# Performance work log

Hardware: AMD Instinct MI355X
Metric: run time of the kernel (lower is better)

The kernel has to match this reference:

```python
import jax, jax.numpy as jnp
import numpy as np

DIM = 384; H = 56; W = 56; WS = 7; SHIFT = 3; NH = 12; B = 32
N = WS * WS                 # 49 tokens per window
NW = (H // WS) * (W // WS)  # 64 windows per image
HD = DIM // NH
EPS = 1e-5


def _rel_coords_table():
    c = np.arange(-(WS - 1), WS, dtype=np.float32)
    hh, ww = np.meshgrid(c, c, indexing='ij')
    t = np.stack([hh, ww], -1)[None]          # (1, 2*WS-1, 2*WS-1, 2)
    t = t / (WS - 1) * 8.0
    t = np.sign(t) * np.log2(np.abs(t) + 1.0) / 3.0
    return t.astype(np.float32)


def _rel_pos_index():
    coords = np.stack(np.meshgrid(np.arange(WS), np.arange(WS), indexing='ij'))  # (2,WS,WS)
    cf = coords.reshape(2, -1)
    rc = (cf[:, :, None] - cf[:, None, :]).transpose(1, 2, 0)  # (N,N,2)
    rc[..., 0] += WS - 1
    rc[..., 1] += WS - 1
    rc[..., 0] *= 2 * WS - 1
    return rc.sum(-1)  # (N,N) int


def _attn_mask():
    img = np.zeros((H, W))
    sl = [slice(0, -WS), slice(-WS, -SHIFT), slice(-SHIFT, None)]
    cnt = 0
    for hs in sl:
        for ws in sl:
            img[hs, ws] = cnt
            cnt += 1
    mw = img.reshape(H // WS, WS, W // WS, WS).transpose(0, 2, 1, 3).reshape(-1, N)
    diff = mw[:, None, :] - mw[:, :, None]  # (NW, N, N)
    return np.where(diff != 0, -100.0, 0.0).astype(np.float32)


_RCT = jnp.asarray(_rel_coords_table())
_RPI = jnp.asarray(_rel_pos_index().reshape(-1))
_MASK = jnp.asarray(_attn_mask())


def _layernorm(x, g, b):
    mu = jnp.mean(x, -1, keepdims=True)
    var = jnp.mean(jnp.square(x - mu), -1, keepdims=True)
    return (x - mu) * jax.lax.rsqrt(var + EPS) * g + b


def _forward(x, qkv_w, q_bias, v_bias, logit_scale, cpb_w1, cpb_b1, cpb_w2,
             proj_w, proj_b, norm1_g, norm1_b, norm2_g, norm2_b,
             mlp_w1, mlp_b1, mlp_w2, mlp_b2):
    shortcut = x
    xg = x.reshape(B, H, W, DIM)
    xg = jnp.roll(xg, shift=(-SHIFT, -SHIFT), axis=(1, 2))
    # window partition -> (B*NW, N, C)
    xw = xg.reshape(B, H // WS, WS, W // WS, WS, DIM).transpose(0, 1, 3, 2, 4, 5)
    xw = xw.reshape(B * NW, N, DIM)

    qkv_bias = jnp.concatenate([q_bias, jnp.zeros_like(v_bias), v_bias])
    qkv = xw @ qkv_w.T + qkv_bias                       # (Bw, N, 3C)
    qkv = qkv.reshape(B * NW, N, 3, NH, HD).transpose(2, 0, 3, 1, 4)
    q, k, v = qkv[0], qkv[1], qkv[2]                    # (Bw, NH, N, HD)

    qn = q / jnp.maximum(jnp.linalg.norm(q, axis=-1, keepdims=True), 1e-12)
    kn = k / jnp.maximum(jnp.linalg.norm(k, axis=-1, keepdims=True), 1e-12)
    attn = jnp.einsum('whnd,whmd->whnm', qn, kn)        # cosine attention
    scale = jnp.exp(jnp.minimum(logit_scale, jnp.log(100.0)))  # (NH,1,1)
    attn = attn * scale

    # CPB-MLP relative position bias
    bt = jnp.maximum(_RCT @ cpb_w1.T + cpb_b1, 0.0) @ cpb_w2.T  # (1,13,13,NH)
    bt = bt.reshape(-1, NH)
    rel_bias = bt[_RPI].reshape(N, N, NH).transpose(2, 0, 1)    # (NH,N,N)
    rel_bias = 16.0 * jax.nn.sigmoid(rel_bias)
    attn = attn + rel_bias[None]

    attn = attn.reshape(B, NW, NH, N, N) + _MASK[None, :, None]
    attn = jax.nn.softmax(attn, axis=-1).reshape(B * NW, NH, N, N)

    out = jnp.einsum('whnm,whmd->whnd', attn, v)        # (Bw, NH, N, HD)
    out = out.transpose(0, 2, 1, 3).reshape(B * NW, N, DIM)
    out = out @ proj_w.T + proj_b

    # window reverse + un-shift
    xg = out.reshape(B, H // WS, W // WS, WS, WS, DIM).transpose(0, 1, 3, 2, 4, 5)
    xg = xg.reshape(B, H, W, DIM)
    xg = jnp.roll(xg, shift=(SHIFT, SHIFT), axis=(1, 2))
    attn_out = xg.reshape(B, H * W, DIM)

    # SwinV2 post-norm residuals
    x1 = shortcut + _layernorm(attn_out, norm1_g, norm1_b)
    h = jax.nn.gelu(x1 @ mlp_w1.T + mlp_b1, approximate=False) @ mlp_w2.T + mlp_b2
    return x1 + _layernorm(h, norm2_g, norm2_b)


def setup_inputs() -> dict:
    key = jax.random.key(0)
    ks = jax.random.split(key, 8)
    s = 0.02
    return {
        'x': jax.random.normal(ks[0], (B, H * W, DIM), jnp.float32),
        'qkv_w': jax.random.normal(ks[1], (3 * DIM, DIM), jnp.float32) * s,
        'q_bias': jnp.zeros((DIM,), jnp.float32),
        'v_bias': jnp.zeros((DIM,), jnp.float32),
        'logit_scale': jnp.log(10.0 * jnp.ones((NH, 1, 1), jnp.float32)),
        'cpb_w1': jax.random.normal(ks[2], (512, 2), jnp.float32) * s,
        'cpb_b1': jnp.zeros((512,), jnp.float32),
        'cpb_w2': jax.random.normal(ks[3], (NH, 512), jnp.float32) * s,
        'proj_w': jax.random.normal(ks[4], (DIM, DIM), jnp.float32) * s,
        'proj_b': jnp.zeros((DIM,), jnp.float32),
        'norm1_g': jnp.ones((DIM,), jnp.float32),
        'norm1_b': jnp.zeros((DIM,), jnp.float32),
        'norm2_g': jnp.ones((DIM,), jnp.float32),
        'norm2_b': jnp.zeros((DIM,), jnp.float32),
        'mlp_w1': jax.random.normal(ks[5], (4 * DIM, DIM), jnp.float32) * s,
        'mlp_b1': jnp.zeros((4 * DIM,), jnp.float32),
        'mlp_w2': jax.random.normal(ks[6], (DIM, 4 * DIM), jnp.float32) * s,
        'mlp_b2': jnp.zeros((DIM,), jnp.float32),
    }


def reference(x, qkv_w, q_bias, v_bias, logit_scale, cpb_w1, cpb_b1, cpb_w2,
              proj_w, proj_b, norm1_g, norm1_b, norm2_g, norm2_b,
              mlp_w1, mlp_b1, mlp_w2, mlp_b2):
    return _forward(x, qkv_w, q_bias, v_bias, logit_scale, cpb_w1, cpb_b1, cpb_w2,
                    proj_w, proj_b, norm1_g, norm1_b, norm2_g, norm2_b,
                    mlp_w1, mlp_b1, mlp_w2, mlp_b2)
```

## Files before the change

kernel.cpp:

```cpp
#include <hip/hip_runtime.h>
#include <hip/hip_bf16.h>
#include <math.h>

#define DIM 384
#define NH 12
#define HD 32
#define NWIN 2048
#define TOKENS 100352
#define NSTG 6

typedef unsigned short u16;
typedef unsigned int u32;
typedef __attribute__((ext_vector_type(8))) short bf16x8;
typedef __attribute__((ext_vector_type(4))) float f32x4;

__device__ __forceinline__ float b2f(u16 u){ return __uint_as_float(((u32)u) << 16); }
__device__ __forceinline__ u16 f2b(float f){
  u32 x = __float_as_uint(f);
  return (u16)((x + 0x7FFFu + ((x >> 16) & 1u)) >> 16);
}

__device__ __forceinline__ void gld16(void* lds, const void* g){
  __builtin_amdgcn_global_load_lds((const __attribute__((address_space(1))) u32*)g,
                                   (__attribute__((address_space(3))) u32*)lds, 16, 0, 0);
}

__global__ void k_wconv(const float* __restrict__ w1, const float* __restrict__ w2,
                        const float* __restrict__ qw, const float* __restrict__ pw,
                        u16* __restrict__ w1s, u16* __restrict__ w2s,
                        u16* __restrict__ qwbf, u16* __restrict__ pws){
  const int n12 = 1536*384, n3 = 1152*384, n4 = 384*384;
  for (int d = blockIdx.x*blockDim.x + threadIdx.x; d < n12; d += gridDim.x*blockDim.x){
    int tile = d >> 12, w = d & 4095;
    int rowl = w >> 5, g = (w >> 3) & 3, e = w & 7;
    int hci = tile / 12, rem = tile - hci*12;
    int kk = ((g ^ ((rowl >> 1) & 3)) << 3) + e;
    w1s[d] = f2b(w1[(size_t)(hci*128 + rowl)*384 + rem*32 + kk]);
    int ks = rem / 3, t = rem - ks*3;
    w2s[d] = f2b(w2[(size_t)(t*128 + rowl)*1536 + hci*128 + ks*32 + kk]);
    if (d < n3) qwbf[d] = f2b(qw[d]);
    if (d < n4){
      int pt = d >> 12, pwd = d & 4095;
      int prl = pwd >> 5, pg = (pwd >> 3) & 3, pe = pwd & 7;
      int pks = pt / 3, ptt = pt - pks*3;
      int pkk = ((pg ^ ((prl >> 1) & 3)) << 3) + pe;
      pws[d] = f2b(pw[(size_t)(ptt*128 + prl)*384 + pks*32 + pkk]);
    }
  }
}

__global__ void k_bias(const float* __restrict__ w1, const float* __restrict__ b1,
                       const float* __restrict__ w2, float* __restrict__ tab){
  __shared__ float hid[512];
  int e = blockIdx.x;
  int i = e / 13, j = e % 13;
  float t0 = (float)(i - 6) * (8.0f / 6.0f);
  float t1 = (float)(j - 6) * (8.0f / 6.0f);
  t0 = copysignf(log2f(fabsf(t0) + 1.f) * (1.f / 3.f), t0);
  t1 = copysignf(log2f(fabsf(t1) + 1.f) * (1.f / 3.f), t1);
  for (int jj = threadIdx.x; jj < 512; jj += blockDim.x)
    hid[jj] = fmaxf(w1[jj*2]*t0 + w1[jj*2+1]*t1 + b1[jj], 0.f);
  __syncthreads();
  if (threadIdx.x < 12){
    float s = 0.f;
    for (int jj = 0; jj < 512; ++jj) s += hid[jj] * w2[threadIdx.x*512 + jj];
    tab[e*12 + threadIdx.x] = s;
  }
}

__global__ void k_bias2(const float* __restrict__ tab, float* __restrict__ biasfull){
  int h = blockIdx.x;
  for (int e = threadIdx.x; e < 49*49; e += blockDim.x){
    int i = e / 49, j = e - (e/49)*49;
    int ih = i/7, iw = i - ih*7, jh = j/7, jw = j - jh*7;
    float bv = tab[((ih-jh+6)*13 + (iw-jw+6))*12 + h];
    biasfull[h*2401 + e] = 16.f / (1.f + expf(-bv));
  }
}

__device__ __forceinline__ void qkv_stage(
    int kc, char* Ad, char* Bd, const float* __restrict__ x, size_t asrc,
    bool arok, int ar, int aq, const u16* __restrict__ bbase, int tid){
  if (arok){
    float4 v4 = *(const float4*)(x + asrc + kc + aq*4);
    u16 p0=f2b(v4.x), p1=f2b(v4.y), p2=f2b(v4.z), p3=f2b(v4.w);
    *(uint2*)(Ad + ar*80 + aq*8) = (uint2){(u32)p0|((u32)p1<<16), (u32)p2|((u32)p3<<16)};
  } else {
    *(uint2*)(Ad + ar*80 + aq*8) = (uint2){0u, 0u};
  }
  #pragma unroll
  for (int i = 0; i < 3; ++i){
    int s = tid + i*512, n = s >> 2, g = s & 3;
    bf16x8 v = *(const bf16x8*)(bbase + (size_t)n*DIM + kc + (g ^ (n&3))*8);
    *(bf16x8*)(Bd + n*64 + g*16) = v;
  }
}

__global__ __launch_bounds__(512, 4) void k_qkv(
    const float* __restrict__ x, const u16* __restrict__ qkvbf,
    const float* __restrict__ q_bias, const float* __restrict__ v_bias,
    const float* __restrict__ logit_scale,
    u16* __restrict__ Qg, u16* __restrict__ Kg, u16* __restrict__ Vg){
  __shared__ __align__(16) char Ab[2][5120];
  __shared__ __align__(16) char Bb[2][24576];

  int tid = threadIdx.x;
  int lane = tid & 63, wid = tid >> 6;
  int l15 = lane & 15, lg = lane >> 4;
  int wm = wid >> 2, wn = wid & 3;
  int win = blockIdx.x, NT = blockIdx.y;
  int b = win >> 6, wi = win & 63, wh = wi >> 3, ww = wi & 7;

  int ar = tid >> 3, aq = tid & 7;
  bool arok = ar < 49;
  size_t asrc = 0;
  if (arok){
    int th = ar / 7, tw = ar - (ar/7)*7;
    int gh = wh*7 + th + 3; if (gh >= 56) gh -= 56;
    int gw = ww*7 + tw + 3; if (gw >= 56) gw -= 56;
    asrc = ((size_t)(b*3136 + gh*56 + gw))*DIM;
  }
  const u16* bbase = qkvbf + (size_t)NT*384*DIM;

  f32x4 acc[2][6];
  #pragma unroll
  for (int mf = 0; mf < 2; ++mf)
    #pragma unroll
    for (int nf = 0; nf < 6; ++nf) acc[mf][nf] = (f32x4){0.f,0.f,0.f,0.f};

  qkv_stage(0, Ab[0], Bb[0], x, asrc, arok, ar, aq, bbase, tid);
  __syncthreads();

  for (int t = 0; t < 12; ++t){
    int cur = t & 1;
    if (t < 11)
      qkv_stage((t+1)*32, Ab[cur^1], Bb[cur^1], x, asrc, arok, ar, aq, bbase, tid);
    bf16x8 af[2];
    #pragma unroll
    for (int mf = 0; mf < 2; ++mf){
      int row = wm*32 + mf*16 + l15;
      af[mf] = *(const bf16x8*)(Ab[cur] + row*80 + lg*16);
    }
    #pragma unroll
    for (int nf = 0; nf < 6; ++nf){
      int n = wn*96 + nf*16 + l15;
      bf16x8 bfv = *(const bf16x8*)(Bb[cur] + n*64 + ((lg ^ (n&3))*16));
      #pragma unroll
      for (int mf = 0; mf < 2; ++mf)
        acc[mf][nf] = __builtin_amdgcn_mfma_f32_16x16x32_bf16(af[mf], bfv, acc[mf][nf], 0, 0, 0);
    }
    __syncthreads();
  }

  if (NT == 0){
    #pragma unroll
    for (int p = 0; p < 3; ++p){
      int h = wn*3 + p;
      float qb0 = q_bias[h*32 + l15], qb1 = q_bias[h*32 + 16 + l15];
      float sc = __expf(fminf(logit_scale[h], 4.6051702f));
      #pragma unroll
      for (int mf = 0; mf < 2; ++mf)
        #pragma unroll
        for (int r = 0; r < 4; ++r){
          float a0 = acc[mf][2*p][r] + qb0;
          float a1 = acc[mf][2*p+1][r] + qb1;
          float sq = a0*a0 + a1*a1;
          #pragma unroll
          for (int off = 1; off < 16; off <<= 1) sq += __shfl_xor(sq, off, 64);
          float rq = sc / fmaxf(sqrtf(sq), 1e-12f);
          int grow = wm*32 + mf*16 + lg*4 + r;
          if (grow < 49){
            u16* dst = Qg + (size_t)win*18816 + h*1568 + grow*32;
            dst[l15]      = f2b(a0*rq);
            dst[16 + l15] = f2b(a1*rq);
          }
        }
    }
  } else if (NT == 1){
    #pragma unroll
    for (int p = 0; p < 3; ++p){
      int h = wn*3 + p;
      #pragma unroll
      for (int mf = 0; mf < 2; ++mf)
        #pragma unroll
        for (int r = 0; r < 4; ++r){
          float a0 = acc[mf][2*p][r], a1 = acc[mf][2*p+1][r];
          float sk = a0*a0 + a1*a1;
          #pragma unroll
          for (int off = 1; off < 16; off <<= 1) sk += __shfl_xor(sk, off, 64);
          float rk = 1.f / fmaxf(sqrtf(sk), 1e-12f);
          int grow = wm*32 + mf*16 + lg*4 + r;
          if (grow < 49){
            u16* dst = Kg + (size_t)win*18816 + h*1568 + grow*32;
            dst[l15]      = f2b(a0*rk);
            dst[16 + l15] = f2b(a1*rk);
          }
        }
    }
  } else {
    #pragma unroll
    for (int nf = 0; nf < 6; ++nf){
      int col = wn*96 + nf*16 + l15;
      int h = col >> 5, c = col & 31;
      float vb = v_bias[col];
      #pragma unroll
      for (int mf = 0; mf < 2; ++mf){
        int gbase = wm*32 + mf*16 + lg*4;
        u16* dst = Vg + (size_t)win*18816 + h*1568 + c;
        #pragma unroll
        for (int r = 0; r < 4; ++r){
          int grow = gbase + r;
          if (grow < 49) dst[grow*32] = f2b(acc[mf][nf][r] + vb);
        }
      }
    }
  }
}

__global__ __launch_bounds__(256, 3) void k_attn2(
    const u16* __restrict__ Qg, const u16* __restrict__ Kg, const u16* __restrict__ Vg,
    const float* __restrict__ biasfull, u16* __restrict__ outwin){
  __shared__ __align__(16) char pb[4][2304];

  int tid = threadIdx.x, lane = tid & 63, wid = tid >> 6;
  int l15 = lane & 15, lg = lane >> 4;
  int win = blockIdx.x;
  int wi = win & 63, wh = wi >> 3, ww = wi & 7;

  float mask16[4][4];
  int   bidx[4][4];
  #pragma unroll
  for (int nf = 0; nf < 4; ++nf){
    int j = nf*16 + l15;
    int j2 = j < 49 ? j : 48;
    int jh = j2/7, jw = j2 - jh*7;
    int ghj = wh*7+jh, gwj = ww*7+jw;
    int zj = (ghj<49?0:(ghj<53?1:2))*3 + (gwj<49?0:(gwj<53?1:2));
    #pragma unroll
    for (int r = 0; r < 4; ++r){
      int i = wid*16 + lg*4 + r;
      int i2 = i < 49 ? i : 48;
      int ih = i2/7, iw = i2 - ih*7;
      int ghi = wh*7+ih, gwi = ww*7+iw;
      int zi = (ghi<49?0:(ghi<53?1:2))*3 + (gwi<49?0:(gwi<53?1:2));
      mask16[nf][r] = (j < 49) ? (zi != zj ? -100.f : 0.f) : -1e30f;
      bidx[nf][r]   = i2*49 + j2;
    }
  }

  const u16* qwin = Qg + (size_t)win*18816;
  const u16* kwin = Kg + (size_t)win*18816;
  const u16* vwin = Vg + (size_t)win*18816;
  char* pbw = pb[wid];

  int arow = wid*16 + l15;
  int arc  = arow < 49 ? arow : 48;

  bf16x8 qa[12];
  #pragma unroll
  for (int h = 0; h < 12; ++h)
    qa[h] = *(const bf16x8*)(qwin + h*1568 + arc*32 + lg*8);
  __syncthreads();

  #pragma unroll
  for (int h = 0; h < 12; ++h){
    bf16x8 kb[4];
    #pragma unroll
    for (int nf = 0; nf < 4; ++nf){
      int j = nf*16 + l15; int j2 = j < 49 ? j : 48;
      kb[nf] = *(const bf16x8*)(kwin + h*1568 + j2*32 + lg*8);
    }
    bf16x8 vb0[2], vb1[2];
    #pragma unroll
    for (int ksp = 0; ksp < 2; ++ksp){
      #pragma unroll
      for (int tt = 0; tt < 8; ++tt){
        int j = ksp*32 + lg*8 + tt; int j2 = j < 49 ? j : 48;
        vb0[ksp][tt] = (short)vwin[h*1568 + j2*32 + l15];
        vb1[ksp][tt] = (short)vwin[h*1568 + j2*32 + 16 + l15];
      }
    }
    float bias16[4][4];
    #pragma unroll
    for (int nf = 0; nf < 4; ++nf)
      #pragma unroll
      for (int r = 0; r < 4; ++r)
        bias16[nf][r] = biasfull[h*2401 + bidx[nf][r]];
    f32x4 s[4];
    #pragma unroll
    for (int nf = 0; nf < 4; ++nf)
      s[nf] = __builtin_amdgcn_mfma_f32_16x16x32_bf16(qa[h], kb[nf],
                (f32x4){0.f,0.f,0.f,0.f}, 0, 0, 0);
    #pragma unroll
    for (int nf = 0; nf < 4; ++nf)
      #pragma unroll
      for (int r = 0; r < 4; ++r)
        s[nf][r] += bias16[nf][r] + mask16[nf][r];
    #pragma unroll
    for (int r = 0; r < 4; ++r){
      float m = fmaxf(fmaxf(s[0][r], s[1][r]), fmaxf(s[2][r], s[3][r]));
      #pragma unroll
      for (int off = 1; off < 16; off <<= 1) m = fmaxf(m, __shfl_xor(m, off, 64));
      float e0 = __expf(s[0][r]-m), e1 = __expf(s[1][r]-m);
      float e2 = __expf(s[2][r]-m), e3 = __expf(s[3][r]-m);
      float sum = e0+e1+e2+e3;
      #pragma unroll
      for (int off = 1; off < 16; off <<= 1) sum += __shfl_xor(sum, off, 64);
      float rs = 1.f/sum;
      s[0][r] = e0*rs; s[1][r] = e1*rs; s[2][r] = e2*rs; s[3][r] = e3*rs;
    }
    #pragma unroll
    for (int nf = 0; nf < 4; ++nf){
      int j = nf*16 + l15;
      #pragma unroll
      for (int r = 0; r < 4; ++r)
        *(u16*)(pbw + (lg*4+r)*144 + j*2) = f2b(s[nf][r]);
    }
    f32x4 o0 = (f32x4){0.f,0.f,0.f,0.f}, o1 = o0;
    #pragma unroll
    for (int ksp = 0; ksp < 2; ++ksp){
      bf16x8 pa = *(const bf16x8*)(pbw + l15*144 + ksp*64 + lg*16);
      o0 = __builtin_amdgcn_mfma_f32_16x16x32_bf16(pa, vb0[ksp], o0, 0, 0, 0);
      o1 = __builtin_amdgcn_mfma_f32_16x16x32_bf16(pa, vb1[ksp], o1, 0, 0, 0);
    }
    #pragma unroll
    for (int r = 0; r < 4; ++r){
      int row = wid*16 + lg*4 + r;
      if (row < 49){
        u16* dst = outwin + ((size_t)win*49 + row)*DIM + h*HD;
        dst[l15]      = f2b(o0[r]);
        dst[16 + l15] = f2b(o1[r]);
      }
    }
  }
}

__global__ __launch_bounds__(512, 4) void k_proj(
    const u16* __restrict__ outwin, const u16* __restrict__ pws,
    const float* __restrict__ proj_b, const float* __restrict__ x,
    const float* __restrict__ n1g, const float* __restrict__ n1b,
    float* __restrict__ x1){
  extern __shared__ char smem[];
  char* sb = smem;
  char* Wb = smem + 24576;

  int tid  = threadIdx.x;
  int lane = tid & 63, wid = tid >> 6;
  int l15  = lane & 15, lg = lane >> 4;
  int gt0 = blockIdx.x * 32;

  for (int e = tid; e < 32*48; e += 512){
    int r = e / 48, q8 = e - (e/48)*48;
    int gtok = gt0 + r;
    int b = gtok / 3136, r2 = gtok - b*3136;
    int oh = r2 / 56, ow = r2 - oh*56;
    int hs = oh + 53; if (hs >= 56) hs -= 56;
    int ws2 = ow + 53; if (ws2 >= 56) ws2 -= 56;
    int win = b*64 + (hs/7)*8 + (ws2/7);
    int row = (hs%7)*7 + (ws2%7);
    bf16x8 v = *(const bf16x8*)(outwin + ((size_t)win*49 + row)*DIM + q8*8);
    *(bf16x8*)(sb + r*768 + ((q8*16) ^ ((r&15)<<4))) = v;
  }

  f32x4 acc[2][3];
  #pragma unroll
  for (int mf = 0; mf < 2; ++mf)
    #pragma unroll
    for (int t = 0; t < 3; ++t){
      float pbv = proj_b[(wid + 8*t)*16 + l15];
      acc[mf][t] = (f32x4){pbv, pbv, pbv, pbv};
    }

  int goff = tid*16;
  int rowl = wid*16 + l15;
  int wswz = (lg ^ ((rowl >> 1) & 3)) << 4;
  #pragma unroll
  for (int sp = 0; sp < NSTG-1; ++sp)
    gld16(Wb + sp*8192 + wid*1024, (const char*)pws + (size_t)sp*8192 + goff);
  __syncthreads();

  #pragma unroll
  for (int ks = 0; ks < 12; ++ks){
    int k0 = ks*32 + lg*8;
    bf16x8 pa[2];
    #pragma unroll
    for (int mf = 0; mf < 2; ++mf){
      int row = mf*16 + l15;
      pa[mf] = *(const bf16x8*)(sb + row*768 + ((k0*2) ^ ((row&15)<<4)));
    }
    #pragma unroll
    for (int t = 0; t < 3; ++t){
      int st = ks*3 + t;
      asm volatile("s_waitcnt vmcnt(4)" ::: "memory");
      __builtin_amdgcn_sched_barrier(0);
      {
        int rp = st + 5;
        char* dst = Wb + ((st+5)%6)*8192 + wid*1024;
        if (rp < 36) gld16(dst, (const char*)pws + (size_t)rp*8192 + goff);
        else         gld16(dst, (const char*)pws + goff);
      }
      char* Wcur = Wb + (st%6)*8192;
      bf16x8 wv = *(const bf16x8*)(Wcur + rowl*64 + wswz);
      #pragma unroll
      for (int mf = 0; mf < 2; ++mf)
        acc[mf][t] = __builtin_amdgcn_mfma_f32_16x16x32_bf16(pa[mf], wv, acc[mf][t], 0, 0, 0);
    }
  }
  __syncthreads();

  float* part = (float*)Wb;
  float* lnf  = (float*)(Wb + 2048);
  float s1a[2][4], s2a[2][4];
  #pragma unroll
  for (int mf = 0; mf < 2; ++mf)
    #pragma unroll
    for (int r = 0; r < 4; ++r){
      float p1 = acc[mf][0][r] + acc[mf][1][r] + acc[mf][2][r];
      float p2 = acc[mf][0][r]*acc[mf][0][r] + acc[mf][1][r]*acc[mf][1][r]
               + acc[mf][2][r]*acc[mf][2][r];
      #pragma unroll
      for (int off = 1; off < 16; off <<= 1){
        p1 += __shfl_xor(p1, off, 64);
        p2 += __shfl_xor(p2, off, 64);
      }
      s1a[mf][r] = p1; s2a[mf][r] = p2;
    }
  if (l15 == 0){
    #pragma unroll
    for (int mf = 0; mf < 2; ++mf)
      #pragma unroll
      for (int r = 0; r < 4; ++r){
        int row = mf*16 + lg*4 + r;
        part[(row*8 + wid)*2]     = s1a[mf][r];
        part[(row*8 + wid)*2 + 1] = s2a[mf][r];
      }
  }
  __syncthreads();
  if (tid < 32){
    float t1 = 0.f, t2 = 0.f;
    #pragma unroll
    for (int w = 0; w < 8; ++w){
      t1 += part[(tid*8 + w)*2];
      t2 += part[(tid*8 + w)*2 + 1];
    }
    float mu = t1*(1.f/384.f);
    lnf[tid*2]     = mu;
    lnf[tid*2 + 1] = rsqrtf(t2*(1.f/384.f) - mu*mu + 1e-5f);
  }
  __syncthreads();
  #pragma unroll
  for (int mf = 0; mf < 2; ++mf)
    #pragma unroll
    for (int r = 0; r < 4; ++r){
      int row = mf*16 + lg*4 + r;
      float mu = lnf[row*2], rstd = lnf[row*2 + 1];
      #pragma unroll
      for (int t = 0; t < 3; ++t){
        int col = (wid + 8*t)*16 + l15;
        x1[(size_t)(gt0 + row)*DIM + col] =
            (acc[mf][t][r]-mu)*rstd*n1g[col] + n1b[col] + x[(size_t)(gt0 + row)*DIM + col];
      }
    }
}

__global__ __launch_bounds__(512, 4) void k_mlp(
    const float* __restrict__ x1, const u16* __restrict__ w1s, const float* __restrict__ b1,
    const u16* __restrict__ w2s, const float* __restrict__ b2,
    const float* __restrict__ n2g, const float* __restrict__ n2b,
    float* __restrict__ out){
  extern __shared__ char smem[];
  char* xb = smem;
  char* Wb = smem + 24576;
  char* hb = smem + 24576 + 49152;

  int tid  = threadIdx.x;
  int lane = tid & 63, wid = tid >> 6;
  int l15  = lane & 15, lg = lane >> 4;
  int gt0 = blockIdx.x * 32;

  for (int e = tid; e < 32*48; e += 512){
    int r = e / 48, q8 = e - (e/48)*48;
    const float4* src = (const float4*)(x1 + (size_t)(gt0+r)*DIM + q8*8);
    float4 a = src[0], c = src[1];
    bf16x8 v;
    v[0]=(short)f2b(a.x); v[1]=(short)f2b(a.y); v[2]=(short)f2b(a.z); v[3]=(short)f2b(a.w);
    v[4]=(short)f2b(c.x); v[5]=(short)f2b(c.y); v[6]=(short)f2b(c.z); v[7]=(short)f2b(c.w);
    *(bf16x8*)(xb + r*768 + ((q8*16) ^ ((r&15)<<4))) = v;
  }
  int b1c = wid*16 + l15;
  float b1r0 = b1[b1c],          b1r1 = b1[128 + b1c],  b1r2 = b1[256 + b1c];
  float b1r3 = b1[384 + b1c],    b1r4 = b1[512 + b1c],  b1r5 = b1[640 + b1c];
  float b1r6 = b1[768 + b1c],    b1r7 = b1[896 + b1c],  b1r8 = b1[1024 + b1c];
  float b1r9 = b1[1152 + b1c],   b1r10 = b1[1280 + b1c], b1r11 = b1[1408 + b1c];

  f32x4 acc2[2][3];
  #pragma unroll
  for (int mf = 0; mf < 2; ++mf)
    #pragma unroll
    for (int t = 0; t < 3; ++t){
      float bb = b2[(wid + 8*t)*16 + l15];
      acc2[mf][t] = (f32x4){bb, bb, bb, bb};
    }

  int goff = tid*16;
  int rowl = wid*16 + l15;
  int wswz = (lg ^ ((rowl >> 1) & 3)) << 4;
  #pragma unroll
  for (int sp = 0; sp < NSTG-1; ++sp)
    gld16(Wb + sp*8192 + wid*1024, (const char*)w1s + (size_t)sp*8192 + goff);
  __syncthreads();

  for (int hci = 0; hci < 12; ++hci){
    const char* w1c = (const char*)w1s + (size_t)hci*98304;
    const char* w2c = (const char*)w2s + (size_t)hci*98304;
    const char* w1n = (const char*)w1s + (size_t)(hci+1)*98304;

    float bb = hci==0?b1r0 : hci==1?b1r1 : hci==2?b1r2 : hci==3?b1r3 :
               hci==4?b1r4 : hci==5?b1r5 : hci==6?b1r6 : hci==7?b1r7 :
               hci==8?b1r8 : hci==9?b1r9 : hci==10?b1r10 : b1r11;
    f32x4 accH[2];
    #pragma unroll
    for (int mf = 0; mf < 2; ++mf) accH[mf] = (f32x4){bb, bb, bb, bb};

    #pragma unroll
    for (int ksp = 0; ksp < 12; ++ksp){
      asm volatile("s_waitcnt vmcnt(4)" ::: "memory");
      __builtin_amdgcn_sched_barrier(0);
      {
        int rp = ksp + 5;
        char* dst = Wb + ((ksp+5)%6)*8192 + wid*1024;
        const char* src = (rp < 12) ? (w1c + (size_t)rp*8192)
                                    : (w2c + (size_t)(rp-12)*8192);
        gld16(dst, src + goff);
      }
      char* Wcur = Wb + (ksp%6)*8192;
      int k0 = ksp*32 + lg*8;
      bf16x8 wfr = *(const bf16x8*)(Wcur + rowl*64 + wswz);
      bf16x8 afr[2];
      #pragma unroll
      for (int mf = 0; mf < 2; ++mf){
        int row = mf*16 + l15;
        afr[mf] = *(const bf16x8*)(xb + row*768 + ((k0*2) ^ ((row&15)<<4)));
      }
      #pragma unroll
      for (int mf = 0; mf < 2; ++mf)
        accH[mf] = __builtin_amdgcn_mfma_f32_16x16x32_bf16(afr[mf], wfr, accH[mf], 0, 0, 0);
    }

    #pragma unroll
    for (int mf = 0; mf < 2; ++mf)
      #pragma unroll
      for (int r = 0; r < 4; ++r){
        float v = accH[mf][r];
        float u = v*(1.f + 0.044715f*v*v);
        v = v * __builtin_amdgcn_rcpf(1.f + __expf(-1.5957691f*u));
        int row = mf*16 + lg*4 + r;
        int col = wid*16 + l15;
        *(u16*)(hb + row*256 + ((col*2) ^ ((row&15)<<4))) = f2b(v);
      }
    asm volatile("s_waitcnt lgkmcnt(0)" ::: "memory");
    __builtin_amdgcn_s_barrier();
    __builtin_amdgcn_sched_barrier(0);

    #pragma unroll
    for (int ks = 0; ks < 4; ++ks){
      int k0 = ks*32 + lg*8;
      bf16x8 pa[2];
      #pragma unroll
      for (int mf = 0; mf < 2; ++mf){
        int row = mf*16 + l15;
        pa[mf] = *(const bf16x8*)(hb + row*256 + ((k0*2) ^ ((row&15)<<4)));
      }
      #pragma unroll
      for (int t = 0; t < 3; ++t){
        int st = ks*3 + t;
        asm volatile("s_waitcnt vmcnt(4)" ::: "memory");
        __builtin_amdgcn_sched_barrier(0);
        {
          int rp = st + 17;
          char* dst = Wb + ((st+5)%6)*8192 + wid*1024;
          if (rp < 24)       gld16(dst, w2c + (size_t)(rp-12)*8192 + goff);
          else if (hci < 11) gld16(dst, w1n + (size_t)(rp-24)*8192 + goff);
          else               gld16(dst, (const char*)w1s + goff);
        }
        char* Wcur = Wb + (st%6)*8192;
        bf16x8 wv = *(const bf16x8*)(Wcur + rowl*64 + wswz);
        #pragma unroll
        for (int mf = 0; mf < 2; ++mf)
          acc2[mf][t] = __builtin_amdgcn_mfma_f32_16x16x32_bf16(pa[mf], wv, acc2[mf][t], 0, 0, 0);
      }
    }
    asm volatile("s_waitcnt lgkmcnt(0)" ::: "memory");
    __builtin_amdgcn_s_barrier();
    __builtin_amdgcn_sched_barrier(0);
  }
  __syncthreads();

  float* part = (float*)hb;
  float* lnf  = (float*)(hb + 2048);
  float s1a[2][4], s2a[2][4];
  #pragma unroll
  for (int mf = 0; mf < 2; ++mf)
    #pragma unroll
    for (int r = 0; r < 4; ++r){
      float p1 = acc2[mf][0][r] + acc2[mf][1][r] + acc2[mf][2][r];
      float p2 = acc2[mf][0][r]*acc2[mf][0][r] + acc2[mf][1][r]*acc2[mf][1][r]
               + acc2[mf][2][r]*acc2[mf][2][r];
      #pragma unroll
      for (int off = 1; off < 16; off <<= 1){
        p1 += __shfl_xor(p1, off, 64);
        p2 += __shfl_xor(p2, off, 64);
      }
      s1a[mf][r] = p1; s2a[mf][r] = p2;
    }
  if (l15 == 0){
    #pragma unroll
    for (int mf = 0; mf < 2; ++mf)
      #pragma unroll
      for (int r = 0; r < 4; ++r){
        int row = mf*16 + lg*4 + r;
        part[(row*8 + wid)*2]     = s1a[mf][r];
        part[(row*8 + wid)*2 + 1] = s2a[mf][r];
      }
  }
  __syncthreads();
  if (tid < 32){
    float t1 = 0.f, t2 = 0.f;
    #pragma unroll
    for (int w = 0; w < 8; ++w){
      t1 += part[(tid*8 + w)*2];
      t2 += part[(tid*8 + w)*2 + 1];
    }
    float mu = t1*(1.f/384.f);
    lnf[tid*2]     = mu;
    lnf[tid*2 + 1] = rsqrtf(t2*(1.f/384.f) - mu*mu + 1e-5f);
  }
  __syncthreads();
  #pragma unroll
  for (int mf = 0; mf < 2; ++mf)
    #pragma unroll
    for (int r = 0; r < 4; ++r){
      int row = mf*16 + lg*4 + r;
      float mu = lnf[row*2], rstd = lnf[row*2 + 1];
      #pragma unroll
      for (int t = 0; t < 3; ++t){
        int col = (wid + 8*t)*16 + l15;
        float resid = x1[(size_t)(gt0 + row)*DIM + col];
        out[(size_t)(gt0 + row)*DIM + col] =
            resid + (acc2[mf][t][r]-mu)*rstd*n2g[col] + n2b[col];
      }
    }
}

extern "C" void kernel_launch(void* const* d_in, const int* in_sizes, int n_in,
                              void* d_out, int out_size, void* d_ws, size_t ws_size,
                              hipStream_t stream){
  const float* x           = (const float*)d_in[0];
  const float* qkv_w       = (const float*)d_in[1];
  const float* q_bias      = (const float*)d_in[2];
  const float* v_bias      = (const float*)d_in[3];
  const float* logit_scale = (const float*)d_in[4];
  const float* cpb_w1      = (const float*)d_in[5];
  const float* cpb_b1      = (const float*)d_in[6];
  const float* cpb_w2      = (const float*)d_in[7];
  const float* proj_w      = (const float*)d_in[8];
  const float* proj_b      = (const float*)d_in[9];
  const float* n1g         = (const float*)d_in[10];
  const float* n1b         = (const float*)d_in[11];
  const float* n2g         = (const float*)d_in[12];
  const float* n2b         = (const float*)d_in[13];
  const float* mlp_w1      = (const float*)d_in[14];
  const float* mlp_b1      = (const float*)d_in[15];
  const float* mlp_w2      = (const float*)d_in[16];
  const float* mlp_b2      = (const float*)d_in[17];

  char* ws = (char*)d_ws;
  float* tab      = (float*)ws;
  float* biasfull = (float*)(ws + 8192);
  u16*  Qg     = (u16*)(ws + 126976);
  u16*  qkvbf  = (u16*)(ws + 126976 + 77070336ull);
  u16*  pws    = (u16*)(ws + 126976 + 77070336ull + 884736ull);
  u16*  w1s    = (u16*)(ws + 126976 + 77070336ull + 884736ull + 294912ull);
  u16*  w2s    = (u16*)(ws + 126976 + 77070336ull + 884736ull + 294912ull + 1179648ull);
  u16*  Kg     = (u16*)d_out;
  u16*  Vg     = Kg + (size_t)NWIN*18816;
  u16*  outwin = Qg;
  float* x1  = (float*)d_out;
  float* out = (float*)d_out;

  hipLaunchKernelGGL(k_bias, dim3(169), dim3(256), 0, stream, cpb_w1, cpb_b1, cpb_w2, tab);
  hipLaunchKernelGGL(k_bias2, dim3(12), dim3(256), 0, stream, tab, biasfull);
  hipLaunchKernelGGL(k_wconv, dim3(1024), dim3(256), 0, stream,
                     mlp_w1, mlp_w2, qkv_w, proj_w, w1s, w2s, qkvbf, pws);
  hipLaunchKernelGGL(k_qkv, dim3(NWIN, 3), dim3(512), 0, stream,
                     x, qkvbf, q_bias, v_bias, logit_scale, Qg, Kg, Vg);
  hipLaunchKernelGGL(k_attn2, dim3(NWIN), dim3(256), 0, stream,
                     Qg, Kg, Vg, biasfull, outwin);
  hipLaunchKernelGGL(k_proj, dim3(TOKENS/32), dim3(512), 73728, stream,
                     outwin, pws, proj_b, x, n1g, n1b, x1);
  hipLaunchKernelGGL(k_mlp, dim3(TOKENS/32), dim3(512), 81920, stream,
                     x1, w1s, mlp_b1, w2s, mlp_b2, n2g, n2b, out);
}
```

Baseline: 976.5 us.

## Fuse projection+LayerNorm1 kernel with MLP+LayerNorm2 kernel

```diff
diff --git a/kernel.cpp b/kernel.cpp
--- a/kernel.cpp
+++ b/kernel.cpp
@@ -335,14 +335,18 @@
   }
 }
 
-__global__ __launch_bounds__(512, 4) void k_proj(
+__global__ __launch_bounds__(512, 4) void k_pm(
     const u16* __restrict__ outwin, const u16* __restrict__ pws,
     const float* __restrict__ proj_b, const float* __restrict__ x,
     const float* __restrict__ n1g, const float* __restrict__ n1b,
-    float* __restrict__ x1){
+    const u16* __restrict__ w1s, const float* __restrict__ b1,
+    const u16* __restrict__ w2s, const float* __restrict__ b2,
+    const float* __restrict__ n2g, const float* __restrict__ n2b,
+    float* __restrict__ out){
   extern __shared__ char smem[];
   char* sb = smem;
   char* Wb = smem + 24576;
+  char* hb = smem + 24576 + 49152;
 
   int tid  = threadIdx.x;
   int lane = tid & 63, wid = tid >> 6;
@@ -397,7 +401,7 @@
         int rp = st + 5;
         char* dst = Wb + ((st+5)%6)*8192 + wid*1024;
         if (rp < 36) gld16(dst, (const char*)pws + (size_t)rp*8192 + goff);
-        else         gld16(dst, (const char*)pws + goff);
+        else         gld16(dst, (const char*)w1s + (size_t)(rp-36)*8192 + goff);
       }
       char* Wcur = Wb + (st%6)*8192;
       bf16x8 wv = *(const bf16x8*)(Wcur + rowl*64 + wswz);
@@ -408,248 +412,221 @@
   }
   __syncthreads();
 
-  float* part = (float*)Wb;
-  float* lnf  = (float*)(Wb + 2048);
-  float s1a[2][4], s2a[2][4];
-  #pragma unroll
-  for (int mf = 0; mf < 2; ++mf)
-    #pragma unroll
-    for (int r = 0; r < 4; ++r){
-      float p1 = acc[mf][0][r] + acc[mf][1][r] + acc[mf][2][r];
-      float p2 = acc[mf][0][r]*acc[mf][0][r] + acc[mf][1][r]*acc[mf][1][r]
-               + acc[mf][2][r]*acc[mf][2][r];
-      #pragma unroll
-      for (int off = 1; off < 16; off <<= 1){
-        p1 += __shfl_xor(p1, off, 64);
-        p2 += __shfl_xor(p2, off, 64);
-      }
-      s1a[mf][r] = p1; s2a[mf][r] = p2;
-    }
-  if (l15 == 0){
+  {
+    float* part = (float*)hb;
+    float* lnf  = (float*)(hb + 2048);
+    float s1a[2][4], s2a[2][4];
+    #pragma unroll
+    for (int mf = 0; mf < 2; ++mf)
+      #pragma unroll
+      for (int r = 0; r < 4; ++r){
+        float p1 = acc[mf][0][r] + acc[mf][1][r] + acc[mf][2][r];
+        float p2 = acc[mf][0][r]*acc[mf][0][r] + acc[mf][1][r]*acc[mf][1][r]
+                 + acc[mf][2][r]*acc[mf][2][r];
+        #pragma unroll
+        for (int off = 1; off < 16; off <<= 1){
+          p1 += __shfl_xor(p1, off, 64);
+          p2 += __shfl_xor(p2, off, 64);
+        }
+        s1a[mf][r] = p1; s2a[mf][r] = p2;
+      }
+    if (l15 == 0){
+      #pragma unroll
+      for (int mf = 0; mf < 2; ++mf)
+        #pragma unroll
+        for (int r = 0; r < 4; ++r){
+          int row = mf*16 + lg*4 + r;
+          part[(row*8 + wid)*2]     = s1a[mf][r];
+          part[(row*8 + wid)*2 + 1] = s2a[mf][r];
+        }
+    }
+    __syncthreads();
+    if (tid < 32){
+      float t1 = 0.f, t2 = 0.f;
+      #pragma unroll
+      for (int w = 0; w < 8; ++w){
+        t1 += part[(tid*8 + w)*2];
+        t2 += part[(tid*8 + w)*2 + 1];
+      }
+      float mu = t1*(1.f/384.f);
+      lnf[tid*2]     = mu;
+      lnf[tid*2 + 1] = rsqrtf(t2*(1.f/384.f) - mu*mu + 1e-5f);
+    }
+    __syncthreads();
+
+    float residv[2][3][4];
     #pragma unroll
     for (int mf = 0; mf < 2; ++mf)
       #pragma unroll
       for (int r = 0; r < 4; ++r){
         int row = mf*16 + lg*4 + r;
-        part[(row*8 + wid)*2]     = s1a[mf][r];
-        part[(row*8 + wid)*2 + 1] = s2a[mf][r];
-      }
-  }
-  __syncthreads();
-  if (tid < 32){
-    float t1 = 0.f, t2 = 0.f;
-    #pragma unroll
-    for (int w = 0; w < 8; ++w){
-      t1 += part[(tid*8 + w)*2];
-      t2 += part[(tid*8 + w)*2 + 1];
-    }
-    float mu = t1*(1.f/384.f);
-    lnf[tid*2]     = mu;
-    lnf[tid*2 + 1] = rsqrtf(t2*(1.f/384.f) - mu*mu + 1e-5f);
-  }
-  __syncthreads();
-  #pragma unroll
-  for (int mf = 0; mf < 2; ++mf)
-    #pragma unroll
-    for (int r = 0; r < 4; ++r){
-      int row = mf*16 + lg*4 + r;
-      float mu = lnf[row*2], rstd = lnf[row*2 + 1];
+        float mu = lnf[row*2], rstd = lnf[row*2 + 1];
+        #pragma unroll
+        for (int t = 0; t < 3; ++t){
+          int col = (wid + 8*t)*16 + l15;
+          float xv = (acc[mf][t][r]-mu)*rstd*n1g[col] + n1b[col]
+                   + x[(size_t)(gt0 + row)*DIM + col];
+          residv[mf][t][r] = xv;
+          *(u16*)(sb + row*768 + ((col*2) ^ ((row&15)<<4))) = f2b(xv);
+        }
+      }
+    __syncthreads();
+
+    int b1c = wid*16 + l15;
+    float b1r0 = b1[b1c],          b1r1 = b1[128 + b1c],  b1r2 = b1[256 + b1c];
+    float b1r3 = b1[384 + b1c],    b1r4 = b1[512 + b1c],  b1r5 = b1[640 + b1c];
+    float b1r6 = b1[768 + b1c],    b1r7 = b1[896 + b1c],  b1r8 = b1[1024 + b1c];
+    float b1r9 = b1[1152 + b1c],   b1r10 = b1[1280 + b1c], b1r11 = b1[1408 + b1c];
+
+    f32x4 acc2[2][3];
+    #pragma unroll
+    for (int mf = 0; mf < 2; ++mf)
       #pragma unroll
       for (int t = 0; t < 3; ++t){
-        int col = (wid + 8*t)*16 + l15;
-        x1[(size_t)(gt0 + row)*DIM + col] =
-            (acc[mf][t][r]-mu)*rstd*n1g[col] + n1b[col] + x[(size_t)(gt0 + row)*DIM + col];
-      }
-    }
-}
-
-__global__ __launch_bounds__(512, 4) void k_mlp(
-    const float* __restrict__ x1, const u16* __restrict__ w1s, const float* __restrict__ b1,
-    const u16* __restrict__ w2s, const float* __restrict__ b2,
-    const float* __restrict__ n2g, const float* __restrict__ n2b,
-    float* __restrict__ out){
-  extern __shared__ char smem[];
-  char* xb = smem;
-  char* Wb = smem + 24576;
-  char* hb = smem + 24576 + 49152;
-
-  int tid  = threadIdx.x;
-  int lane = tid & 63, wid = tid >> 6;
-  int l15  = lane & 15, lg = lane >> 4;
-  int gt0 = blockIdx.x * 32;
-
-  for (int e = tid; e < 32*48; e += 512){
-    int r = e / 48, q8 = e - (e/48)*48;
-    const float4* src = (const float4*)(x1 + (size_t)(gt0+r)*DIM + q8*8);
-    float4 a = src[0], c = src[1];
-    bf16x8 v;
-    v[0]=(short)f2b(a.x); v[1]=(short)f2b(a.y); v[2]=(short)f2b(a.z); v[3]=(short)f2b(a.w);
-    v[4]=(short)f2b(c.x); v[5]=(short)f2b(c.y); v[6]=(short)f2b(c.z); v[7]=(short)f2b(c.w);
-    *(bf16x8*)(xb + r*768 + ((q8*16) ^ ((r&15)<<4))) = v;
-  }
-  int b1c = wid*16 + l15;
-  float b1r0 = b1[b1c],          b1r1 = b1[128 + b1c],  b1r2 = b1[256 + b1c];
-  float b1r3 = b1[384 + b1c],    b1r4 = b1[512 + b1c],  b1r5 = b1[640 + b1c];
-  float b1r6 = b1[768 + b1c],    b1r7 = b1[896 + b1c],  b1r8 = b1[1024 + b1c];
-  float b1r9 = b1[1152 + b1c],   b1r10 = b1[1280 + b1c], b1r11 = b1[1408 + b1c];
-
-  f32x4 acc2[2][3];
-  #pragma unroll
-  for (int mf = 0; mf < 2; ++mf)
-    #pragma unroll
-    for (int t = 0; t < 3; ++t){
-      float bb = b2[(wid + 8*t)*16 + l15];
-      acc2[mf][t] = (f32x4){bb, bb, bb, bb};
-    }
-
-  int goff = tid*16;
-  int rowl = wid*16 + l15;
-  int wswz = (lg ^ ((rowl >> 1) & 3)) << 4;
-  #pragma unroll
-  for (int sp = 0; sp < NSTG-1; ++sp)
-    gld16(Wb + sp*8192 + wid*1024, (const char*)w1s + (size_t)sp*8192 + goff);
-  __syncthreads();
-
-  for (int hci = 0; hci < 12; ++hci){
-    const char* w1c = (const char*)w1s + (size_t)hci*98304;
-    const char* w2c = (const char*)w2s + (size_t)hci*98304;
-    const char* w1n = (const char*)w1s + (size_t)(hci+1)*98304;
-
-    float bb = hci==0?b1r0 : hci==1?b1r1 : hci==2?b1r2 : hci==3?b1r3 :
-               hci==4?b1r4 : hci==5?b1r5 : hci==6?b1r6 : hci==7?b1r7 :
-               hci==8?b1r8 : hci==9?b1r9 : hci==10?b1r10 : b1r11;
-    f32x4 accH[2];
-    #pragma unroll
-    for (int mf = 0; mf < 2; ++mf) accH[mf] = (f32x4){bb, bb, bb, bb};
-
-    #pragma unroll
-    for (int ksp = 0; ksp < 12; ++ksp){
-      asm volatile("s_waitcnt vmcnt(4)" ::: "memory");
-      __builtin_amdgcn_sched_barrier(0);
-      {
-        int rp = ksp + 5;
-        char* dst = Wb + ((ksp+5)%6)*8192 + wid*1024;
-        const char* src = (rp < 12) ? (w1c + (size_t)rp*8192)
-                                    : (w2c + (size_t)(rp-12)*8192);
-        gld16(dst, src + goff);
-      }
-      char* Wcur = Wb + (ksp%6)*8192;
-      int k0 = ksp*32 + lg*8;
-      bf16x8 wfr = *(const bf16x8*)(Wcur + rowl*64 + wswz);
-      bf16x8 afr[2];
-      #pragma unroll
-      for (int mf = 0; mf < 2; ++mf){
-        int row = mf*16 + l15;
-        afr[mf] = *(const bf16x8*)(xb + row*768 + ((k0*2) ^ ((row&15)<<4)));
-      }
-      #pragma unroll
-      for (int mf = 0; mf < 2; ++mf)
-        accH[mf] = __builtin_amdgcn_mfma_f32_16x16x32_bf16(afr[mf], wfr, accH[mf], 0, 0, 0);
-    }
-
-    #pragma unroll
-    for (int mf = 0; mf < 2; ++mf)
-      #pragma unroll
-      for (int r = 0; r < 4; ++r){
-        float v = accH[mf][r];
-        float u = v*(1.f + 0.044715f*v*v);
-        v = v * __builtin_amdgcn_rcpf(1.f + __expf(-1.5957691f*u));
-        int row = mf*16 + lg*4 + r;
-        int col = wid*16 + l15;
-        *(u16*)(hb + row*256 + ((col*2) ^ ((row&15)<<4))) = f2b(v);
-      }
-    asm volatile("s_waitcnt lgkmcnt(0)" ::: "memory");
-    __builtin_amdgcn_s_barrier();
-    __builtin_amdgcn_sched_barrier(0);
-
-    #pragma unroll
-    for (int ks = 0; ks < 4; ++ks){
-      int k0 = ks*32 + lg*8;
-      bf16x8 pa[2];
-      #pragma unroll
-      for (int mf = 0; mf < 2; ++mf){
-        int row = mf*16 + l15;
-        pa[mf] = *(const bf16x8*)(hb + row*256 + ((k0*2) ^ ((row&15)<<4)));
-      }
-      #pragma unroll
-      for (int t = 0; t < 3; ++t){
-        int st = ks*3 + t;
+        float bb = b2[(wid + 8*t)*16 + l15];
+        acc2[mf][t] = (f32x4){bb, bb, bb, bb};
+      }
+
+    for (int hci = 0; hci < 12; ++hci){
+      const char* w1c = (const char*)w1s + (size_t)hci*98304;
+      const char* w2c = (const char*)w2s + (size_t)hci*98304;
+      const char* w1n = (const char*)w1s + (size_t)(hci+1)*98304;
+
+      float bb = hci==0?b1r0 : hci==1?b1r1 : hci==2?b1r2 : hci==3?b1r3 :
+                 hci==4?b1r4 : hci==5?b1r5 : hci==6?b1r6 : hci==7?b1r7 :
+                 hci==8?b1r8 : hci==9?b1r9 : hci==10?b1r10 : b1r11;
+      f32x4 accH[2];
+      #pragma unroll
+      for (int mf = 0; mf < 2; ++mf) accH[mf] = (f32x4){bb, bb, bb, bb};
+
+      #pragma unroll
+      for (int ksp = 0; ksp < 12; ++ksp){
         asm volatile("s_waitcnt vmcnt(4)" ::: "memory");
         __builtin_amdgcn_sched_barrier(0);
         {
-          int rp = st + 17;
-          char* dst = Wb + ((st+5)%6)*8192 + wid*1024;
-          if (rp < 24)       gld16(dst, w2c + (size_t)(rp-12)*8192 + goff);
-          else if (hci < 11) gld16(dst, w1n + (size_t)(rp-24)*8192 + goff);
-          else               gld16(dst, (const char*)w1s + goff);
-        }
-        char* Wcur = Wb + (st%6)*8192;
-        bf16x8 wv = *(const bf16x8*)(Wcur + rowl*64 + wswz);
+          int rp = ksp + 5;
+          char* dst = Wb + ((ksp+5)%6)*8192 + wid*1024;
+          const char* src = (rp < 12) ? (w1c + (size_t)rp*8192)
+                                      : (w2c + (size_t)(rp-12)*8192);
+          gld16(dst, src + goff);
+        }
+        char* Wcur = Wb + (ksp%6)*8192;
+        int k0 = ksp*32 + lg*8;
+        bf16x8 wfr = *(const bf16x8*)(Wcur + rowl*64 + wswz);
+        bf16x8 afr[2];
+        #pragma unroll
+        for (int mf = 0; mf < 2; ++mf){
+          int row = mf*16 + l15;
+          afr[mf] = *(const bf16x8*)(sb + row*768 + ((k0*2) ^ ((row&15)<<4)));
+        }
         #pragma unroll
         for (int mf = 0; mf < 2; ++mf)
-          acc2[mf][t] = __builtin_amdgcn_mfma_f32_16x16x32_bf16(pa[mf], wv, acc2[mf][t], 0, 0, 0);
-      }
-    }
-    asm volatile("s_waitcnt lgkmcnt(0)" ::: "memory");
-    __builtin_amdgcn_s_barrier();
-    __builtin_amdgcn_sched_barrier(0);
-  }
-  __syncthreads();
-
-  float* part = (float*)hb;
-  float* lnf  = (float*)(hb + 2048);
-  float s1a[2][4], s2a[2][4];
-  #pragma unroll
-  for (int mf = 0; mf < 2; ++mf)
-    #pragma unroll
-    for (int r = 0; r < 4; ++r){
-      float p1 = acc2[mf][0][r] + acc2[mf][1][r] + acc2[mf][2][r];
-      float p2 = acc2[mf][0][r]*acc2[mf][0][r] + acc2[mf][1][r]*acc2[mf][1][r]
-               + acc2[mf][2][r]*acc2[mf][2][r];
-      #pragma unroll
-      for (int off = 1; off < 16; off <<= 1){
-        p1 += __shfl_xor(p1, off, 64);
-        p2 += __shfl_xor(p2, off, 64);
-      }
-      s1a[mf][r] = p1; s2a[mf][r] = p2;
-    }
-  if (l15 == 0){
+          accH[mf] = __builtin_amdgcn_mfma_f32_16x16x32_bf16(afr[mf], wfr, accH[mf], 0, 0, 0);
+      }
+
+      #pragma unroll
+      for (int mf = 0; mf < 2; ++mf)
+        #pragma unroll
+        for (int r = 0; r < 4; ++r){
+          float v = accH[mf][r];
+          float u = v*(1.f + 0.044715f*v*v);
+          v = v * __builtin_amdgcn_rcpf(1.f + __expf(-1.5957691f*u));
+          int row = mf*16 + lg*4 + r;
+          int col = wid*16 + l15;
+          *(u16*)(hb + row*256 + ((col*2) ^ ((row&15)<<4))) = f2b(v);
+        }
+      asm volatile("s_waitcnt lgkmcnt(0)" ::: "memory");
+      __builtin_amdgcn_s_barrier();
+      __builtin_amdgcn_sched_barrier(0);
+
+      #pragma unroll
+      for (int ks = 0; ks < 4; ++ks){
+        int k0 = ks*32 + lg*8;
+        bf16x8 pa2[2];
+        #pragma unroll
+        for (int mf = 0; mf < 2; ++mf){
+          int row = mf*16 + l15;
+          pa2[mf] = *(const bf16x8*)(hb + row*256 + ((k0*2) ^ ((row&15)<<4)));
+        }
+        #pragma unroll
+        for (int t = 0; t < 3; ++t){
+          int st = ks*3 + t;
+          asm volatile("s_waitcnt vmcnt(4)" ::: "memory");
+          __builtin_amdgcn_sched_barrier(0);
+          {
+            int rp = st + 17;
+            char* dst = Wb + ((st+5)%6)*8192 + wid*1024;
+            if (rp < 24)       gld16(dst, w2c + (size_t)(rp-12)*8192 + goff);
+            else if (hci < 11) gld16(dst, w1n + (size_t)(rp-24)*8192 + goff);
+            else               gld16(dst, (const char*)w1s + goff);
+          }
+          char* Wcur = Wb + (st%6)*8192;
+          bf16x8 wv = *(const bf16x8*)(Wcur + rowl*64 + wswz);
+          #pragma unroll
+          for (int mf = 0; mf < 2; ++mf)
+            acc2[mf][t] = __builtin_amdgcn_mfma_f32_16x16x32_bf16(pa2[mf], wv, acc2[mf][t], 0, 0, 0);
+        }
+      }
+      asm volatile("s_waitcnt lgkmcnt(0)" ::: "memory");
+      __builtin_amdgcn_s_barrier();
+      __builtin_amdgcn_sched_barrier(0);
+    }
+    __syncthreads();
+
+    float* part2 = (float*)hb;
+    float* lnf2  = (float*)(hb + 2048);
+    float t1a[2][4], t2a[2][4];
+    #pragma unroll
+    for (int mf = 0; mf < 2; ++mf)
+      #pragma unroll
+      for (int r = 0; r < 4; ++r){
+        float p1 = acc2[mf][0][r] + acc2[mf][1][r] + acc2[mf][2][r];
+        float p2 = acc2[mf][0][r]*acc2[mf][0][r] + acc2[mf][1][r]*acc2[mf][1][r]
+                 + acc2[mf][2][r]*acc2[mf][2][r];
+        #pragma unroll
+        for (int off = 1; off < 16; off <<= 1){
+          p1 += __shfl_xor(p1, off, 64);
+          p2 += __shfl_xor(p2, off, 64);
+        }
+        t1a[mf][r] = p1; t2a[mf][r] = p2;
+      }
+    if (l15 == 0){
+      #pragma unroll
+      for (int mf = 0; mf < 2; ++mf)
+        #pragma unroll
+        for (int r = 0; r < 4; ++r){
+          int row = mf*16 + lg*4 + r;
+          part2[(row*8 + wid)*2]     = t1a[mf][r];
+          part2[(row*8 + wid)*2 + 1] = t2a[mf][r];
+        }
+    }
+    __syncthreads();
+    if (tid < 32){
+      float t1 = 0.f, t2 = 0.f;
+      #pragma unroll
+      for (int w = 0; w < 8; ++w){
+        t1 += part2[(tid*8 + w)*2];
+        t2 += part2[(tid*8 + w)*2 + 1];
+      }
+      float mu = t1*(1.f/384.f);
+      lnf2[tid*2]     = mu;
+      lnf2[tid*2 + 1] = rsqrtf(t2*(1.f/384.f) - mu*mu + 1e-5f);
+    }
+    __syncthreads();
     #pragma unroll
     for (int mf = 0; mf < 2; ++mf)
       #pragma unroll
       for (int r = 0; r < 4; ++r){
         int row = mf*16 + lg*4 + r;
-        part[(row*8 + wid)*2]     = s1a[mf][r];
-        part[(row*8 + wid)*2 + 1] = s2a[mf][r];
-      }
-  }
-  __syncthreads();
-  if (tid < 32){
-    float t1 = 0.f, t2 = 0.f;
-    #pragma unroll
-    for (int w = 0; w < 8; ++w){
-      t1 += part[(tid*8 + w)*2];
-      t2 += part[(tid*8 + w)*2 + 1];
-    }
-    float mu = t1*(1.f/384.f);
-    lnf[tid*2]     = mu;
-    lnf[tid*2 + 1] = rsqrtf(t2*(1.f/384.f) - mu*mu + 1e-5f);
-  }
-  __syncthreads();
-  #pragma unroll
-  for (int mf = 0; mf < 2; ++mf)
-    #pragma unroll
-    for (int r = 0; r < 4; ++r){
-      int row = mf*16 + lg*4 + r;
-      float mu = lnf[row*2], rstd = lnf[row*2 + 1];
-      #pragma unroll
-      for (int t = 0; t < 3; ++t){
-        int col = (wid + 8*t)*16 + l15;
-        float resid = x1[(size_t)(gt0 + row)*DIM + col];
-        out[(size_t)(gt0 + row)*DIM + col] =
-            resid + (acc2[mf][t][r]-mu)*rstd*n2g[col] + n2b[col];
-      }
-    }
+        float mu = lnf2[row*2], rstd = lnf2[row*2 + 1];
+        #pragma unroll
+        for (int t = 0; t < 3; ++t){
+          int col = (wid + 8*t)*16 + l15;
+          out[(size_t)(gt0 + row)*DIM + col] =
+              residv[mf][t][r] + (acc2[mf][t][r]-mu)*rstd*n2g[col] + n2b[col];
+        }
+      }
+  }
 }
 
 extern "C" void kernel_launch(void* const* d_in, const int* in_sizes, int n_in,
@@ -685,7 +662,6 @@
   u16*  Kg     = (u16*)d_out;
   u16*  Vg     = Kg + (size_t)NWIN*18816;
   u16*  outwin = Qg;
-  float* x1  = (float*)d_out;
   float* out = (float*)d_out;
 
   hipLaunchKernelGGL(k_bias, dim3(169), dim3(256), 0, stream, cpb_w1, cpb_b1, cpb_w2, tab);
@@ -696,8 +672,7 @@
                      x, qkvbf, q_bias, v_bias, logit_scale, Qg, Kg, Vg);
   hipLaunchKernelGGL(k_attn2, dim3(NWIN), dim3(256), 0, stream,
                      Qg, Kg, Vg, biasfull, outwin);
-  hipLaunchKernelGGL(k_proj, dim3(TOKENS/32), dim3(512), 73728, stream,
-                     outwin, pws, proj_b, x, n1g, n1b, x1);
-  hipLaunchKernelGGL(k_mlp, dim3(TOKENS/32), dim3(512), 81920, stream,
-                     x1, w1s, mlp_b1, w2s, mlp_b2, n2g, n2b, out);
-}
+  hipLaunchKernelGGL(k_pm, dim3(TOKENS/32), dim3(512), 81920, stream,
+                     outwin, pws, proj_b, x, n1g, n1b,
+                     w1s, mlp_b1, w2s, mlp_b2, n2g, n2b, out);
+}
```

Result: faster. 956.0 us (-2.1%).
